# Kernel tuning notes

Hardware: AMD Instinct MI355X
Metric: run time of the kernel (lower is better)

## Reference

```python
import jax, jax.numpy as jnp
import numpy as np

N, D, P = 4096, 1024, 2048
TAU, ALPHA = 0.2, 0.8
GAMMA_EX, GAMMA_IN = 2.0, 1.6
EPS = 1e-8


def _cos_sim(e):
    # F.cosine_similarity(e[:,None], e[None,:], dim=2) == normalized rows matmul
    n = jnp.linalg.norm(e, axis=1, keepdims=True)
    en = e / jnp.maximum(n, EPS)
    return en @ en.T  # [N, N]


def setup_inputs() -> dict:
    key = jax.random.key(0)
    embeddings = jax.random.normal(key, (N, D), dtype=jnp.float32)
    # positive pairs: (0,1),(2,3),... (arange fill)
    pp = np.arange(2 * P).reshape(P, 2)
    pos_partner = np.arange(N)
    pos_partner[pp[:, 0]] = pp[:, 1]
    pos_partner[pp[:, 1]] = pp[:, 0]
    # negative pairs = all ordered (i,j), i!=j, minus ordered positive tuples,
    # enumerated row-major (deterministic stand-in for torch's set order).
    pos_m = np.zeros((N, N), dtype=bool)
    pos_m[pp[:, 0], pp[:, 1]] = True
    neg_m = ~np.eye(N, dtype=bool) & ~pos_m
    ii, jj = np.nonzero(neg_m)  # row-major order
    neg_partner = np.arange(N)
    neg_partner[ii] = jj
    neg_partner[jj] = ii  # processed[j] = ... overwrites after
    return {
        "embeddings": embeddings,
        "positive_pairs": jnp.asarray(pp, jnp.int32),
        "pos_partner": jnp.asarray(pos_partner, jnp.int32),
        "neg_partner": jnp.asarray(neg_partner, jnp.int32),
    }


def reference(embeddings, positive_pairs, pos_partner, neg_partner):
    pi, pj = positive_pairs[:, 0], positive_pairs[:, 1]
    # Beta(gamma,gamma) scalar mixing coefficients (dim_mixing=False)
    lam_pos = jax.random.beta(jax.random.key(1), GAMMA_EX, GAMMA_EX) + 1.0  # 'ex'
    lam_neg = jax.random.beta(jax.random.key(2), GAMMA_IN, GAMMA_IN)        # 'in'

    orig = _cos_sim(embeddings)
    hp = _cos_sim(lam_pos * embeddings + (1.0 - lam_pos) * embeddings[pos_partner])
    hn = _cos_sim(lam_neg * embeddings + (1.0 - lam_neg) * embeddings[neg_partner])

    eye = jnp.eye(N, dtype=bool)
    pos_m = jnp.zeros((N, N), dtype=bool).at[pi, pj].set(True)  # ordered positives
    neg_m = ~eye & ~pos_m                                        # ordered negatives
    # pos replacement first, then neg replacement overwrites (faithful ordering)
    sim = jnp.where(pos_m | pos_m.T, hp, orig)
    sim = jnp.where(neg_m | neg_m.T, hn, sim)

    # ----- compute_loss (stage='train': quantile hard-negative mining) -----
    mask = eye | pos_m | pos_m.T
    exp_sim = jnp.exp(sim / TAU)
    exp_masked = jnp.where(mask, 0.0, exp_sim)
    pos_ij = exp_sim[pi, pj]
    pos_ji = exp_sim[pj, pi]
    exp_i = exp_masked[pi]  # [P, N]
    exp_j = exp_masked[pj]
    thr_i = jnp.quantile(exp_i, ALPHA, axis=1, keepdims=True)
    thr_j = jnp.quantile(exp_j, ALPHA, axis=1, keepdims=True)
    sum_i = jnp.where(exp_i >= thr_i, exp_i, 0.0).sum(axis=1)
    sum_j = jnp.where(exp_j >= thr_j, exp_j, 0.0).sum(axis=1)
    loss_ij = -jnp.log(pos_ij / (pos_ij + sum_i))
    loss_ji = -jnp.log(pos_ji / (pos_ji + sum_j))
    return (loss_ij + loss_ji).sum() / (2 * P)
```

## Files before the change

### kernel.cpp

```cpp
#include <hip/hip_runtime.h>
#include <hip/hip_bf16.h>

#define NN 4096
#define DD 1024
constexpr float LAM = 0.45f;
constexpr float INV_TAU = 5.0f;
constexpr int KSEL = 820;
constexpr unsigned KEY_BASE = 0x3B80u;
constexpr int NBINS = 2048;

typedef __attribute__((ext_vector_type(8))) short bf16x8;
typedef __attribute__((ext_vector_type(4))) float f32x4;

__device__ inline void async_copy16(const ushort* g, ushort* l) {
    __builtin_amdgcn_global_load_lds(
        (const __attribute__((address_space(1))) void*)g,
        (__attribute__((address_space(3))) void*)l, 16, 0, 0);
}

__global__ __launch_bounds__(256) void mixnorm_kernel(const float* __restrict__ E,
                                                      const int* __restrict__ negp,
                                                      ushort* __restrict__ U) {
    int r = blockIdx.x, t = threadIdx.x;
    int p = negp[r];
    const float a = LAM, b = 1.0f - LAM;
    float4 x = ((const float4*)(E + (size_t)r * DD))[t];
    float4 y = ((const float4*)(E + (size_t)p * DD))[t];
    float4 m;
    m.x = a * x.x + b * y.x;
    m.y = a * x.y + b * y.y;
    m.z = a * x.z + b * y.z;
    m.w = a * x.w + b * y.w;
    float ss = m.x * m.x + m.y * m.y + m.z * m.z + m.w * m.w;
    #pragma unroll
    for (int off = 32; off > 0; off >>= 1) ss += __shfl_down(ss, off, 64);
    __shared__ float part[4];
    if ((t & 63) == 0) part[t >> 6] = ss;
    __syncthreads();
    float tot = part[0] + part[1] + part[2] + part[3];
    float inv = 1.0f / fmaxf(sqrtf(tot), 1e-8f);
    ushort4 o;
    o.x = __bfloat16_as_ushort(__float2bfloat16(m.x * inv));
    o.y = __bfloat16_as_ushort(__float2bfloat16(m.y * inv));
    o.z = __bfloat16_as_ushort(__float2bfloat16(m.z * inv));
    o.w = __bfloat16_as_ushort(__float2bfloat16(m.w * inv));
    ((ushort4*)(U + (size_t)r * DD))[t] = o;
}

__global__ __launch_bounds__(512) void gemm_exp_kernel(const ushort* __restrict__ U,
                                                       ushort* __restrict__ Z) {
    __shared__ ushort sm_all[32768];
    const int t = threadIdx.x;
    const int w = t >> 6, l = t & 63;

    const int m = blockIdx.x;
    float fdec = sqrtf(8.0f * (float)m + 1.0f);
    int by = (int)((fdec - 1.0f) * 0.5f);
    while ((by + 1) * (by + 2) / 2 <= m) by++;
    while (by * (by + 1) / 2 > m) by--;
    const int bx = m - by * (by + 1) / 2;

    const int cg = (t & 3) ^ ((t >> 3) & 3);
    const ushort* gA = U + (size_t)(by * 128 + (t >> 2)) * DD + cg * 8;
    const ushort* gB = U + (size_t)(bx * 128 + (t >> 2)) * DD + cg * 8;

    f32x4 acc[2][4];
    #pragma unroll
    for (int i = 0; i < 2; i++)
        #pragma unroll
        for (int j = 0; j < 4; j++) acc[i][j] = (f32x4){0.f, 0.f, 0.f, 0.f};

    const int wr = w >> 1, wc = w & 1;
    const int mrow = wr * 32 + (l & 15);
    const int nrow = wc * 64 + (l & 15);
    const int kqs = ((l >> 4) ^ (((l & 15) >> 1) & 3)) * 8;

    {
        ushort* base = sm_all;
        async_copy16(gA,      base + w * 512);
        async_copy16(gA + 32, base + 4096 + w * 512);
        async_copy16(gB,      base + 8192 + w * 512);
        async_copy16(gB + 32, base + 12288 + w * 512);
    }

    int cur = 0;
    for (int kt = 0; kt < 16; kt++) {
        if (kt < 15) {
            const ushort* ga = gA + (kt + 1) * 64;
            const ushort* gb = gB + (kt + 1) * 64;
            ushort* base = sm_all + (cur ^ 1) * 16384;
            async_copy16(ga,      base + w * 512);
            async_copy16(ga + 32, base + 4096 + w * 512);
            async_copy16(gb,      base + 8192 + w * 512);
            async_copy16(gb + 32, base + 12288 + w * 512);
            asm volatile("s_waitcnt vmcnt(4)" ::: "memory");
        } else {
            asm volatile("s_waitcnt vmcnt(0)" ::: "memory");
        }
        __builtin_amdgcn_s_barrier();
        asm volatile("" ::: "memory");
        const ushort* Abase = sm_all + cur * 16384;
        const ushort* Bbase = Abase + 8192;
        #pragma unroll
        for (int kh = 0; kh < 2; kh++) {
            const ushort* Ah = Abase + kh * 4096;
            const ushort* Bh = Bbase + kh * 4096;
            bf16x8 af[2], bfr[4];
            #pragma unroll
            for (int i = 0; i < 2; i++)
                af[i] = *(const bf16x8*)(Ah + (mrow + i * 16) * 32 + kqs);
            #pragma unroll
            for (int j = 0; j < 4; j++)
                bfr[j] = *(const bf16x8*)(Bh + (nrow + j * 16) * 32 + kqs);
            #pragma unroll
            for (int i = 0; i < 2; i++)
                #pragma unroll
                for (int j = 0; j < 4; j++)
                    acc[i][j] = __builtin_amdgcn_mfma_f32_16x16x32_bf16(af[i], bfr[j], acc[i][j], 0, 0, 0);
        }
        asm volatile("" ::: "memory");
        __builtin_amdgcn_s_barrier();
        cur ^= 1;
    }

    ushort* smv = sm_all;
    ushort* smT = sm_all + 4096;
    const bool mirror = (bx != by);
    #pragma unroll
    for (int h = 0; h < 4; h++) {
        __syncthreads();
        if (wr == h) {
            #pragma unroll
            for (int i = 0; i < 2; i++)
                #pragma unroll
                for (int j = 0; j < 4; j++)
                    #pragma unroll
                    for (int rg = 0; rg < 4; rg++) {
                        float v = __expf(acc[i][j][rg] * INV_TAU);
                        ushort hv = __bfloat16_as_ushort(__float2bfloat16(v));
                        int lrow = i * 16 + ((l >> 4) << 2) + rg;
                        int lcol = (wc << 6) + j * 16 + (l & 15);
                        smv[lrow * 128 + lcol] = hv;
                        smT[lcol * 48 + lrow] = hv;
                    }
        }
        __syncthreads();
        {
            const uint4* src = (const uint4*)(smv + (t >> 4) * 128 + (t & 15) * 8);
            uint4* dst = (uint4*)(Z + (size_t)(by * 128 + h * 32 + (t >> 4)) * NN + bx * 128 + (t & 15) * 8);
            *dst = *src;
        }
        if (mirror) {
            const uint4* srcT = (const uint4*)(smT + (t >> 2) * 48 + (t & 3) * 8);
            uint4* dstT = (uint4*)(Z + (size_t)(bx * 128 + (t >> 2)) * NN + by * 128 + h * 32 + (t & 3) * 8);
            *dstT = *srcT;
        }
    }
}

__global__ __launch_bounds__(256) void rowloss_kernel(const ushort* __restrict__ Z,
                                                      const int* __restrict__ posp,
                                                      float* __restrict__ loss) {
    const int t = threadIdx.x, w = t >> 6, l = t & 63;
    const int r = blockIdx.x * 4 + w;
    const int p = posp[r];
    const uint4* zr = (const uint4*)(Z + (size_t)r * NN);

    const float posv = __uint_as_float(((unsigned)Z[(size_t)r * NN + p]) << 16);

    unsigned ko[32];
    #pragma unroll
    for (int c = 0; c < 8; c++) {
        uint4 v = zr[c * 64 + l];
        unsigned wd[4] = {v.x, v.y, v.z, v.w};
        const int cb = (c * 64 + l) * 8;
        #pragma unroll
        for (int q = 0; q < 4; q++) {
            int c0 = cb + 2 * q, c1 = c0 + 1;
            unsigned x = wd[q];
            unsigned klo = (c0 == p || c0 == r) ? 0u : (x & 0xFFFFu);
            unsigned khi = (c1 == p || c1 == r) ? 0u : (x >> 16);
            ko[c * 4 + q] = klo | (khi << 16) | 0x80008000u;
        }
    }

    unsigned lo_b = KEY_BASE, hi_b = KEY_BASE + NBINS;
    #pragma unroll 1
    for (int it = 0; it < 11; it++) {
        unsigned mid = (lo_b + hi_b) >> 1;
        unsigned mm = mid | (mid << 16);
        unsigned a = 0;
        #pragma unroll
        for (int i = 0; i < 32; i++)
            a += ((ko[i] - mm) >> 15) & 0x10001u;
        #pragma unroll
        for (int d = 1; d < 64; d <<= 1) a += __shfl_xor(a, d, 64);
        unsigned c = (a & 0xFFFFu) + (a >> 16);
        bool ge = (c >= (unsigned)KSEL);
        lo_b = ge ? mid : lo_b;
        hi_b = ge ? hi_b : mid;
    }
    const unsigned thr = lo_b;

    float s0 = 0.f, s1 = 0.f;
    #pragma unroll
    for (int i = 0; i < 32; i++) {
        unsigned x = ko[i] & 0x7FFF7FFFu;
        unsigned klo = x & 0xFFFFu;
        unsigned khi = x >> 16;
        float vlo = __uint_as_float(klo << 16);
        float vhi = __uint_as_float(x & 0xFFFF0000u);
        s0 += (klo >= thr) ? vlo : 0.f;
        s1 += (khi >= thr) ? vhi : 0.f;
    }
    float s = s0 + s1;
    #pragma unroll
    for (int d = 1; d < 64; d <<= 1) s += __shfl_xor(s, d, 64);
    if (l == 0) loss[r] = log1pf(s / posv);
}

__global__ __launch_bounds__(256) void finalize_kernel(const float* __restrict__ loss,
                                                       unsigned* __restrict__ out) {
    __shared__ float part[4];
    const int t = threadIdx.x, w = t >> 6, l = t & 63;
    float s = 0.f;
    #pragma unroll
    for (int q = 0; q < 4; q++) {
        float4 v = ((const float4*)loss)[t * 4 + q];
        s += (v.x + v.y) + (v.z + v.w);
    }
    #pragma unroll
    for (int off = 32; off > 0; off >>= 1) s += __shfl_down(s, off, 64);
    if (l == 0) part[w] = s;
    __syncthreads();
    if (t == 0) {
        float v = (part[0] + part[1] + part[2] + part[3]) * (1.0f / 4096.0f);
        unsigned short bits = __bfloat16_as_ushort(__float2bfloat16(v));
        *out = ((unsigned)bits << 16) | (unsigned)bits;
    }
}

extern "C" void kernel_launch(void* const* d_in, const int* in_sizes, int n_in,
                              void* d_out, int out_size, void* d_ws, size_t ws_size,
                              hipStream_t stream) {
    const float* E = (const float*)d_in[0];
    const int* posp = (const int*)d_in[2];
    const int* negp = (const int*)d_in[3];

    float* loss = (float*)d_ws;
    ushort* U = (ushort*)((char*)d_ws + 16384);
    ushort* Z = (ushort*)((char*)d_ws + 16384 + (size_t)NN * DD * 2);

    mixnorm_kernel<<<NN, 256, 0, stream>>>(E, negp, U);
    gemm_exp_kernel<<<528, 512, 0, stream>>>(U, Z);
    rowloss_kernel<<<NN / 4, 256, 0, stream>>>(Z, posp, loss);
    finalize_kernel<<<1, 256, 0, stream>>>(loss, (unsigned*)d_out);
}
```

Measured before the change: 124.1 us.

## Split GEMM tiles into 64-row halves and swizzle block order across XCDs

The symmetric GEMM+exp kernel now launches 1056 blocks of 256 threads, each computing a 64x128 half of a lower-triangular 128x128 tile instead of one full tile per 512-thread block. Block IDs are remapped so consecutive IDs land on the same XCD group (bid&7 stride mapping), aiming for better L2 reuse of shared B tiles. Shared memory per block drops, which should allow more resident blocks and better load balance across CUs. The cost is that the B operand is loaded twice per full tile, and the epilogue needs more store iterations per thread.

```diff
diff --git a/kernel.cpp b/kernel.cpp
--- a/kernel.cpp
+++ b/kernel.cpp
@@ -47,22 +47,29 @@
     ((ushort4*)(U + (size_t)r * DD))[t] = o;
 }
 
-__global__ __launch_bounds__(512) void gemm_exp_kernel(const ushort* __restrict__ U,
+__global__ __launch_bounds__(256) void gemm_exp_kernel(const ushort* __restrict__ U,
                                                        ushort* __restrict__ Z) {
-    __shared__ ushort sm_all[32768];
+    __shared__ ushort sm_all[24576];
     const int t = threadIdx.x;
     const int w = t >> 6, l = t & 63;
 
-    const int m = blockIdx.x;
-    float fdec = sqrtf(8.0f * (float)m + 1.0f);
+    const int bid = blockIdx.x;
+    const int m2 = (bid & 7) * 132 + (bid >> 3);
+    const int tri = m2 >> 1, hb = m2 & 1;
+
+    float fdec = sqrtf(8.0f * (float)tri + 1.0f);
     int by = (int)((fdec - 1.0f) * 0.5f);
-    while ((by + 1) * (by + 2) / 2 <= m) by++;
-    while (by * (by + 1) / 2 > m) by--;
-    const int bx = m - by * (by + 1) / 2;
+    while ((by + 1) * (by + 2) / 2 <= tri) by++;
+    while (by * (by + 1) / 2 > tri) by--;
+    const int bx = tri - by * (by + 1) / 2;
+
+    const int row0 = by * 128 + hb * 64;
+    const int col0 = bx * 128;
 
     const int cg = (t & 3) ^ ((t >> 3) & 3);
-    const ushort* gA = U + (size_t)(by * 128 + (t >> 2)) * DD + cg * 8;
-    const ushort* gB = U + (size_t)(bx * 128 + (t >> 2)) * DD + cg * 8;
+    const ushort* gA = U + (size_t)(row0 + (t >> 2)) * DD + cg * 8;
+    const ushort* gB = U + (size_t)(col0 + (t >> 2)) * DD + cg * 8;
+    const size_t bstep = (size_t)64 * DD;
 
     f32x4 acc[2][4];
     #pragma unroll
@@ -75,35 +82,35 @@
     const int nrow = wc * 64 + (l & 15);
     const int kqs = ((l >> 4) ^ (((l & 15) >> 1) & 3)) * 8;
 
-    {
-        ushort* base = sm_all;
-        async_copy16(gA,      base + w * 512);
-        async_copy16(gA + 32, base + 4096 + w * 512);
-        async_copy16(gB,      base + 8192 + w * 512);
-        async_copy16(gB + 32, base + 12288 + w * 512);
-    }
+    #define STAGE(base_, ko_)                                                   \
+        do {                                                                    \
+            ushort* base = (base_);                                             \
+            const int ko = (ko_);                                               \
+            async_copy16(gA + ko,               base + w * 512);                \
+            async_copy16(gA + ko + 32,          base + 2048 + w * 512);         \
+            async_copy16(gB + ko,               base + 4096 + w * 512);         \
+            async_copy16(gB + bstep + ko,       base + 6144 + w * 512);         \
+            async_copy16(gB + ko + 32,          base + 8192 + w * 512);         \
+            async_copy16(gB + bstep + ko + 32,  base + 10240 + w * 512);        \
+        } while (0)
+
+    STAGE(sm_all, 0);
 
     int cur = 0;
     for (int kt = 0; kt < 16; kt++) {
         if (kt < 15) {
-            const ushort* ga = gA + (kt + 1) * 64;
-            const ushort* gb = gB + (kt + 1) * 64;
-            ushort* base = sm_all + (cur ^ 1) * 16384;
-            async_copy16(ga,      base + w * 512);
-            async_copy16(ga + 32, base + 4096 + w * 512);
-            async_copy16(gb,      base + 8192 + w * 512);
-            async_copy16(gb + 32, base + 12288 + w * 512);
-            asm volatile("s_waitcnt vmcnt(4)" ::: "memory");
+            STAGE(sm_all + (cur ^ 1) * 12288, (kt + 1) * 64);
+            asm volatile("s_waitcnt vmcnt(6)" ::: "memory");
         } else {
             asm volatile("s_waitcnt vmcnt(0)" ::: "memory");
         }
         __builtin_amdgcn_s_barrier();
         asm volatile("" ::: "memory");
-        const ushort* Abase = sm_all + cur * 16384;
-        const ushort* Bbase = Abase + 8192;
+        const ushort* Abase = sm_all + cur * 12288;
+        const ushort* Bbase = Abase + 4096;
         #pragma unroll
         for (int kh = 0; kh < 2; kh++) {
-            const ushort* Ah = Abase + kh * 4096;
+            const ushort* Ah = Abase + kh * 2048;
             const ushort* Bh = Bbase + kh * 4096;
             bf16x8 af[2], bfr[4];
             #pragma unroll
@@ -122,12 +129,13 @@
         __builtin_amdgcn_s_barrier();
         cur ^= 1;
     }
+    #undef STAGE
 
     ushort* smv = sm_all;
     ushort* smT = sm_all + 4096;
     const bool mirror = (bx != by);
     #pragma unroll
-    for (int h = 0; h < 4; h++) {
+    for (int h = 0; h < 2; h++) {
         __syncthreads();
         if (wr == h) {
             #pragma unroll
@@ -146,14 +154,26 @@
         }
         __syncthreads();
         {
-            const uint4* src = (const uint4*)(smv + (t >> 4) * 128 + (t & 15) * 8);
-            uint4* dst = (uint4*)(Z + (size_t)(by * 128 + h * 32 + (t >> 4)) * NN + bx * 128 + (t & 15) * 8);
-            *dst = *src;
+            #pragma unroll
+            for (int c = 0; c < 2; c++) {
+                int idx = c * 256 + t;
+                int row = idx >> 4;
+                int col8 = idx & 15;
+                const uint4* src = (const uint4*)(smv + row * 128 + col8 * 8);
+                uint4* dst = (uint4*)(Z + (size_t)(row0 + h * 32 + row) * NN + col0 + col8 * 8);
+                *dst = *src;
+            }
         }
         if (mirror) {
-            const uint4* srcT = (const uint4*)(smT + (t >> 2) * 48 + (t & 3) * 8);
-            uint4* dstT = (uint4*)(Z + (size_t)(bx * 128 + (t >> 2)) * NN + by * 128 + h * 32 + (t & 3) * 8);
-            *dstT = *srcT;
+            #pragma unroll
+            for (int c = 0; c < 2; c++) {
+                int idx = c * 256 + t;
+                int row = idx >> 2;
+                int col8 = idx & 3;
+                const uint4* srcT = (const uint4*)(smT + row * 48 + col8 * 8);
+                uint4* dstT = (uint4*)(Z + (size_t)(col0 + row) * NN + row0 + h * 32 + col8 * 8);
+                *dstT = *srcT;
+            }
         }
     }
 }
@@ -252,7 +272,7 @@
     ushort* Z = (ushort*)((char*)d_ws + 16384 + (size_t)NN * DD * 2);
 
     mixnorm_kernel<<<NN, 256, 0, stream>>>(E, negp, U);
-    gemm_exp_kernel<<<528, 512, 0, stream>>>(U, Z);
+    gemm_exp_kernel<<<1056, 256, 0, stream>>>(U, Z);
     rowloss_kernel<<<NN / 4, 256, 0, stream>>>(Z, posp, loss);
     finalize_kernel<<<1, 256, 0, stream>>>(loss, (unsigned*)d_out);
 }
```

Result: no change. 123.8 us (-0.2%).
